# Kernel optimization log

Measured on AMD Instinct MI355X. Metric: run time of the kernel, lower is better.

## Reference

```python
import jax, jax.numpy as jnp
import numpy as np

NUM_HEADS = 12

def setup_inputs() -> dict:
    key = jax.random.key(0)
    k1, k2, k3 = jax.random.split(key, 3)
    B, N, C = 2, 4096, 768
    x = jax.random.normal(k1, (B, N, C), dtype=jnp.float32)
    w_qkv = jax.random.normal(k2, (C, 3 * C), dtype=jnp.float32) * 0.02
    b_qkv = jnp.zeros((3 * C,), dtype=jnp.float32)
    w_proj = jax.random.normal(k3, (C, C), dtype=jnp.float32) * 0.02
    b_proj = jnp.zeros((C,), dtype=jnp.float32)
    return {"x": x, "w_qkv": w_qkv, "b_qkv": b_qkv, "w_proj": w_proj, "b_proj": b_proj}

def reference(x, w_qkv, b_qkv, w_proj, b_proj):
    B, N, C = x.shape
    H = NUM_HEADS
    D = C // H
    # fused QKV projection: [B,N,3C] -> [B,N,3,H,D] -> [3,B,H,N,D]
    qkv = (x @ w_qkv + b_qkv).reshape(B, N, 3, H, D).transpose(2, 0, 3, 1, 4)
    q, k, v = qkv[0], qkv[1], qkv[2]
    # unnormalized (softmax-free) attention, same op order as the torch module
    attn = jnp.einsum('bhnd,bhmd->bhnm', q, k) / jnp.sqrt(jnp.float32(D))  # [B,H,N,N]
    out = jnp.einsum('bhnm,bhmd->bhnd', attn, v)  # [B,H,N,D]
    out = out.transpose(0, 2, 1, 3).reshape(B, N, C)
    return out @ w_proj + b_proj
```

## Files before the change

### kernel.cpp

```cpp
#include <hip/hip_runtime.h>

typedef unsigned short ushort_t;
typedef __bf16 bf16_t;
typedef __attribute__((ext_vector_type(8))) bf16_t bf16x8;
typedef __attribute__((ext_vector_type(4))) float f32x4;

__device__ __forceinline__ ushort_t f2bf(float f) {
  unsigned int u = __builtin_bit_cast(unsigned int, f);
  u += 0x7FFFu + ((u >> 16) & 1u);
  return (ushort_t)(u >> 16);
}

__device__ __forceinline__ float bf2f(ushort_t s) {
  return __builtin_bit_cast(float, (unsigned int)s << 16);
}

__device__ __forceinline__ f32x4 mfma16(bf16x8 a, bf16x8 b, f32x4 c) {
  return __builtin_amdgcn_mfma_f32_16x16x32_bf16(a, b, c, 0, 0, 0);
}

__device__ __forceinline__ void async_copy16(const void* g, void* l) {
  __builtin_amdgcn_global_load_lds(
      (const __attribute__((address_space(1))) unsigned int*)g,
      (__attribute__((address_space(3))) unsigned int*)l,
      16, 0, 0);
}

#define BARRIER { __builtin_amdgcn_s_barrier(); asm volatile("" ::: "memory"); }
#define VMW3 asm volatile("s_waitcnt vmcnt(3)" ::: "memory")
#define VMW0 asm volatile("s_waitcnt vmcnt(0)" ::: "memory")

__global__ __launch_bounds__(256) void conv_all_k(const float* __restrict__ x,
                                                  const float* __restrict__ w,
                                                  ushort_t* __restrict__ xb,
                                                  ushort_t* __restrict__ wqt,
                                                  ushort_t* __restrict__ wqr) {
  __shared__ float lds[64][65];
  const int bid = blockIdx.x;
  const int tid = threadIdx.x;
  if (bid < 3072) {
    int i = (bid * 256 + tid) * 8;
    float4 f0 = *(const float4*)(x + i);
    float4 f1 = *(const float4*)(x + i + 4);
    union { ushort_t s[8]; uint4 v; } u;
    u.s[0] = f2bf(f0.x); u.s[1] = f2bf(f0.y); u.s[2] = f2bf(f0.z); u.s[3] = f2bf(f0.w);
    u.s[4] = f2bf(f1.x); u.s[5] = f2bf(f1.y); u.s[6] = f2bf(f1.z); u.s[7] = f2bf(f1.w);
    *(uint4*)(xb + i) = u.v;
  } else if (bid < 3360) {
    const int ii = bid - 3072;
    const int n0 = 768 + (ii % 24) * 64;
    const int k0 = (ii / 24) * 64;
#pragma unroll
    for (int q = 0; q < 16; ++q) {
      int lin = tid + q * 256;
      int i = lin >> 6, j = lin & 63;
      lds[i][j] = w[(size_t)(k0 + i) * 2304 + n0 + j];
    }
    __syncthreads();
#pragma unroll
    for (int q = 0; q < 16; ++q) {
      int lin = tid + q * 256;
      int jj = lin >> 6, kk = lin & 63;
      wqt[(size_t)(n0 + jj) * 768 + k0 + kk] = f2bf(lds[kk][jj]);
    }
  } else {
    int i = ((bid - 3360) * 256 + tid) * 8;
    int row = i / 768, col = i % 768;
    const float* src = w + (size_t)row * 2304 + col;
    float4 f0 = *(const float4*)src;
    float4 f1 = *(const float4*)(src + 4);
    union { ushort_t s[8]; uint4 v; } u;
    u.s[0] = f2bf(f0.x); u.s[1] = f2bf(f0.y); u.s[2] = f2bf(f0.z); u.s[3] = f2bf(f0.w);
    u.s[4] = f2bf(f1.x); u.s[5] = f2bf(f1.y); u.s[6] = f2bf(f1.z); u.s[7] = f2bf(f1.w);
    *(uint4*)(wqr + i) = u.v;
  }
}

template <bool OUT_BF16>
__global__ __launch_bounds__(512, 2) void g256x192_k(
    const ushort_t* __restrict__ A, int lda, long long sA,
    const ushort_t* __restrict__ Bt, int ldb, long long sB,
    const float* __restrict__ bias, long long sBias,
    void* __restrict__ Cp, int ldc, long long sC,
    int K, int ntiles) {
  __shared__ char smem[114688];
  const int tid = threadIdx.x;
  const int lane = tid & 63;
  const int wid = tid >> 6;
  const int l15 = lane & 15, lhi = lane >> 4;
  const int wr = wid >> 2, wc = wid & 3;
  const int sx = l15 & 7;

  const int nwg = gridDim.x;
  const int q = nwg >> 3;
  const int swz = (blockIdx.x & 7) * q + (blockIdx.x >> 3);
  const int mt = swz / ntiles, nt = swz % ntiles;
  const int m0 = mt << 8, n0 = nt * 192;
  const long long z = blockIdx.y;

  const ushort_t* Ab = A + z * sA;
  const ushort_t* Bb = Bt + z * sB;

  const int r0 = tid >> 3;
  const int sg = tid & 7;
  const int soff = (sg ^ (r0 & 7)) << 4;

#define STAGE_A(BUF, H, K0)                                                      \
  { const char* g0 = (const char*)(Ab + (size_t)(m0 + (H)*128 + r0) * lda + (K0)) + soff;      \
    const char* g1 = (const char*)(Ab + (size_t)(m0 + (H)*128 + r0 + 64) * lda + (K0)) + soff; \
    char* lb = smem + (BUF)*57344 + (H)*16384;                                   \
    async_copy16(g0, lb + tid * 16);                                             \
    async_copy16(g1, lb + 8192 + tid * 16); }

#define STAGE_B3(BUF, J, K0)                                                     \
  { const char* g0 = (const char*)(Bb + (size_t)(n0 + (J)*64 + r0) * ldb + (K0)) + soff;       \
    async_copy16(g0, smem + (BUF)*57344 + 32768 + (J)*8192 + tid * 16); }

  const int aBase = wr * 16384 + l15 * 128;
  const int bBase = 32768 + (wc * 48 + l15) * 128;
  const int sk0 = ((lhi ^ sx) << 4);
  const int sk1 = (((4 + lhi) ^ sx) << 4);

  f32x4 acc[8][3] = {};
  bf16x8 bfr[3][2];

#define DS_A(BUF, MPAIR, AF)                                                     \
  _Pragma("unroll") for (int mm = 0; mm < 2; ++mm) {                             \
    AF[mm][0] = *(const bf16x8*)(smem + (BUF)*57344 + aBase + ((MPAIR)*2+mm)*2048 + sk0); \
    AF[mm][1] = *(const bf16x8*)(smem + (BUF)*57344 + aBase + ((MPAIR)*2+mm)*2048 + sk1); }

#define DS_B(BUF)                                                                \
  _Pragma("unroll") for (int n = 0; n < 3; ++n) {                                \
    bfr[n][0] = *(const bf16x8*)(smem + (BUF)*57344 + bBase + n*2048 + sk0);     \
    bfr[n][1] = *(const bf16x8*)(smem + (BUF)*57344 + bBase + n*2048 + sk1); }

#define MFMA_PH(MPAIR, AF)                                                       \
  __builtin_amdgcn_s_setprio(1);                                                 \
  _Pragma("unroll") for (int mm = 0; mm < 2; ++mm)                               \
    _Pragma("unroll") for (int n = 0; n < 3; ++n) {                              \
      acc[(MPAIR)*2+mm][n] = mfma16(AF[mm][0], bfr[n][0], acc[(MPAIR)*2+mm][n]); \
      acc[(MPAIR)*2+mm][n] = mfma16(AF[mm][1], bfr[n][1], acc[(MPAIR)*2+mm][n]); } \
  __builtin_amdgcn_s_setprio(0);

  STAGE_A(0, 0, 0) STAGE_A(0, 1, 0)
  STAGE_B3(0, 0, 0) STAGE_B3(0, 1, 0) STAGE_B3(0, 2, 0)
  STAGE_B3(1, 0, 64) STAGE_B3(1, 1, 64) STAGE_B3(1, 2, 64)
  VMW3;
  BARRIER

  const int NIT = K >> 7;
#pragma unroll 1
  for (int it = 0; it < NIT - 1; ++it) {
    const int kA = (it << 7) + 64;
    const int k2 = (it << 7) + 128;
    const int k3 = (it << 7) + 192;
    { bf16x8 af[2][2]; DS_B(0) DS_A(0, 0, af) STAGE_A(1, 0, kA)
      BARRIER MFMA_PH(0, af) BARRIER }
    { bf16x8 af[2][2]; DS_A(0, 1, af) STAGE_A(1, 1, kA)
      BARRIER MFMA_PH(1, af) BARRIER }
    { bf16x8 af[2][2]; DS_A(0, 2, af) STAGE_B3(0, 0, k2) STAGE_B3(0, 1, k2)
      BARRIER MFMA_PH(2, af) BARRIER }
    { bf16x8 af[2][2]; DS_A(0, 3, af) STAGE_B3(0, 2, k2) VMW3;
      BARRIER MFMA_PH(3, af) BARRIER }
    { bf16x8 af[2][2]; DS_B(1) DS_A(1, 0, af) STAGE_A(0, 0, k2)
      BARRIER MFMA_PH(0, af) BARRIER }
    { bf16x8 af[2][2]; DS_A(1, 1, af) STAGE_A(0, 1, k2)
      BARRIER MFMA_PH(1, af) BARRIER }
    { bf16x8 af[2][2]; DS_A(1, 2, af) STAGE_B3(1, 0, k3) STAGE_B3(1, 1, k3)
      BARRIER MFMA_PH(2, af) BARRIER }
    { bf16x8 af[2][2]; DS_A(1, 3, af) STAGE_B3(1, 2, k3) VMW3;
      BARRIER MFMA_PH(3, af) BARRIER }
  }
  {
    const int kA = ((NIT - 1) << 7) + 64;
    { bf16x8 af[2][2]; DS_B(0) DS_A(0, 0, af) STAGE_A(1, 0, kA)
      BARRIER MFMA_PH(0, af) BARRIER }
    { bf16x8 af[2][2]; DS_A(0, 1, af) STAGE_A(1, 1, kA)
      BARRIER MFMA_PH(1, af) BARRIER }
    { bf16x8 af[2][2]; DS_A(0, 2, af)
      BARRIER MFMA_PH(2, af) BARRIER }
    { bf16x8 af[2][2]; DS_A(0, 3, af) VMW0;
      BARRIER MFMA_PH(3, af) BARRIER }
    { bf16x8 af[2][2]; DS_B(1) DS_A(1, 0, af)
      BARRIER MFMA_PH(0, af) BARRIER }
    { bf16x8 af[2][2]; DS_A(1, 1, af)
      BARRIER MFMA_PH(1, af) BARRIER }
    { bf16x8 af[2][2]; DS_A(1, 2, af)
      BARRIER MFMA_PH(2, af) BARRIER }
    { bf16x8 af[2][2]; DS_A(1, 3, af)
      BARRIER MFMA_PH(3, af) BARRIER }
  }

  float bv[3];
#pragma unroll
  for (int n = 0; n < 3; ++n) bv[n] = bias[z * sBias + n0 + wc * 48 + n * 16 + l15];
#pragma unroll
  for (int m = 0; m < 8; ++m) {
#pragma unroll
    for (int n = 0; n < 3; ++n) {
#pragma unroll
      for (int ri = 0; ri < 4; ++ri) {
        int row = m0 + wr * 128 + m * 16 + lhi * 4 + ri;
        int col = n0 + wc * 48 + n * 16 + l15;
        float v = acc[m][n][ri] + bv[n];
        size_t ci = (size_t)z * sC + (size_t)row * ldc + col;
        if (OUT_BF16) ((ushort_t*)Cp)[ci] = f2bf(v);
        else          ((float*)Cp)[ci]    = v;
      }
    }
  }
#undef STAGE_A
#undef STAGE_B3
#undef DS_A
#undef DS_B
#undef MFMA_PH
}

template <bool OUT_BF16>
__global__ __launch_bounds__(512, 2) void g128x192_k(
    const ushort_t* __restrict__ A, int lda, long long sA,
    const ushort_t* __restrict__ Bt, int ldb, long long sB,
    const float* __restrict__ bias, long long sBias,
    void* __restrict__ Cp, int ldc, long long sC,
    int K, int ntiles) {
  __shared__ char smem[81920];
  const int tid = threadIdx.x;
  const int lane = tid & 63;
  const int wid = tid >> 6;
  const int l15 = lane & 15, lhi = lane >> 4;
  const int wr = wid >> 2, wc = wid & 3;
  const int sx = l15 & 7;

  const int nwg = gridDim.x;
  const int q = nwg >> 3;
  const int swz = (blockIdx.x & 7) * q + (blockIdx.x >> 3);
  const int mt = swz / ntiles, nt = swz % ntiles;
  const int m0 = mt << 7, n0 = nt * 192;
  const long long z = blockIdx.y;

  const ushort_t* Ab = A + z * sA;
  const ushort_t* Bb = Bt + z * sB;

  const int r0 = tid >> 3;
  const int sg = tid & 7;
  const int soff = (sg ^ (r0 & 7)) << 4;

#define STAGE_A1(BUF, K0)                                                        \
  { const char* g0 = (const char*)(Ab + (size_t)(m0 + r0) * lda + (K0)) + soff;               \
    const char* g1 = (const char*)(Ab + (size_t)(m0 + r0 + 64) * lda + (K0)) + soff;          \
    char* lb = smem + (BUF)*40960;                                               \
    async_copy16(g0, lb + tid * 16);                                             \
    async_copy16(g1, lb + 8192 + tid * 16); }

#define STAGE_B3(BUF, J, K0)                                                     \
  { const char* g0 = (const char*)(Bb + (size_t)(n0 + (J)*64 + r0) * ldb + (K0)) + soff;       \
    async_copy16(g0, smem + (BUF)*40960 + 16384 + (J)*8192 + tid * 16); }

  const int aBase = wr * 8192 + l15 * 128;
  const int bBase = 16384 + (wc * 48 + l15) * 128;
  const int sk0 = ((lhi ^ sx) << 4);
  const int sk1 = (((4 + lhi) ^ sx) << 4);

  f32x4 acc[4][3] = {};
  bf16x8 bfr[3][2];

#define DS_A1(BUF, M, AF)                                                        \
  { AF[0] = *(const bf16x8*)(smem + (BUF)*40960 + aBase + (M)*2048 + sk0);       \
    AF[1] = *(const bf16x8*)(smem + (BUF)*40960 + aBase + (M)*2048 + sk1); }

#define DS_B1(BUF)                                                               \
  _Pragma("unroll") for (int n = 0; n < 3; ++n) {                                \
    bfr[n][0] = *(const bf16x8*)(smem + (BUF)*40960 + bBase + n*2048 + sk0);     \
    bfr[n][1] = *(const bf16x8*)(smem + (BUF)*40960 + bBase + n*2048 + sk1); }

#define MFMA_PH1(M, AF)                                                          \
  __builtin_amdgcn_s_setprio(1);                                                 \
  _Pragma("unroll") for (int n = 0; n < 3; ++n) {                                \
    acc[M][n] = mfma16(AF[0], bfr[n][0], acc[M][n]);                             \
    acc[M][n] = mfma16(AF[1], bfr[n][1], acc[M][n]); }                           \
  __builtin_amdgcn_s_setprio(0);

  STAGE_A1(0, 0)
  STAGE_B3(0, 0, 0) STAGE_B3(0, 1, 0) STAGE_B3(0, 2, 0)
  STAGE_B3(1, 0, 64) STAGE_B3(1, 1, 64) STAGE_B3(1, 2, 64)
  VMW3;
  BARRIER

  const int NIT = K >> 7;
#pragma unroll 1
  for (int it = 0; it < NIT - 1; ++it) {
    const int kA = (it << 7) + 64;
    const int k2 = (it << 7) + 128;
    const int k3 = (it << 7) + 192;
    { bf16x8 af[2]; DS_B1(0) DS_A1(0, 0, af) STAGE_A1(1, kA)
      BARRIER MFMA_PH1(0, af) BARRIER }
    { bf16x8 af[2]; DS_A1(0, 1, af)
      BARRIER MFMA_PH1(1, af) BARRIER }
    { bf16x8 af[2]; DS_A1(0, 2, af) STAGE_B3(0, 0, k2) STAGE_B3(0, 1, k2)
      BARRIER MFMA_PH1(2, af) BARRIER }
    { bf16x8 af[2]; DS_A1(0, 3, af) STAGE_B3(0, 2, k2) VMW3;
      BARRIER MFMA_PH1(3, af) BARRIER }
    { bf16x8 af[2]; DS_B1(1) DS_A1(1, 0, af) STAGE_A1(0, k2)
      BARRIER MFMA_PH1(0, af) BARRIER }
    { bf16x8 af[2]; DS_A1(1, 1, af)
      BARRIER MFMA_PH1(1, af) BARRIER }
    { bf16x8 af[2]; DS_A1(1, 2, af) STAGE_B3(1, 0, k3) STAGE_B3(1, 1, k3)
      BARRIER MFMA_PH1(2, af) BARRIER }
    { bf16x8 af[2]; DS_A1(1, 3, af) STAGE_B3(1, 2, k3) VMW3;
      BARRIER MFMA_PH1(3, af) BARRIER }
  }
  {
    const int kA = ((NIT - 1) << 7) + 64;
    { bf16x8 af[2]; DS_B1(0) DS_A1(0, 0, af) STAGE_A1(1, kA)
      BARRIER MFMA_PH1(0, af) BARRIER }
    { bf16x8 af[2]; DS_A1(0, 1, af)
      BARRIER MFMA_PH1(1, af) BARRIER }
    { bf16x8 af[2]; DS_A1(0, 2, af)
      BARRIER MFMA_PH1(2, af) BARRIER }
    { bf16x8 af[2]; DS_A1(0, 3, af) VMW0;
      BARRIER MFMA_PH1(3, af) BARRIER }
    { bf16x8 af[2]; DS_B1(1) DS_A1(1, 0, af)
      BARRIER MFMA_PH1(0, af) BARRIER }
    { bf16x8 af[2]; DS_A1(1, 1, af)
      BARRIER MFMA_PH1(1, af) BARRIER }
    { bf16x8 af[2]; DS_A1(1, 2, af)
      BARRIER MFMA_PH1(2, af) BARRIER }
    { bf16x8 af[2]; DS_A1(1, 3, af)
      BARRIER MFMA_PH1(3, af) BARRIER }
  }

  float bv[3];
#pragma unroll
  for (int n = 0; n < 3; ++n) bv[n] = bias[z * sBias + n0 + wc * 48 + n * 16 + l15];
#pragma unroll
  for (int m = 0; m < 4; ++m) {
#pragma unroll
    for (int n = 0; n < 3; ++n) {
#pragma unroll
      for (int ri = 0; ri < 4; ++ri) {
        int row = m0 + wr * 64 + m * 16 + lhi * 4 + ri;
        int col = n0 + wc * 48 + n * 16 + l15;
        float v = acc[m][n][ri] + bv[n];
        size_t ci = (size_t)z * sC + (size_t)row * ldc + col;
        if (OUT_BF16) ((ushort_t*)Cp)[ci] = f2bf(v);
        else          ((float*)Cp)[ci]    = v;
      }
    }
  }
#undef STAGE_A1
#undef STAGE_B3
#undef DS_A1
#undef DS_B1
#undef MFMA_PH1
}

__global__ __launch_bounds__(256) void kv_k(const ushort_t* __restrict__ kv,
                                            float* __restrict__ Sp) {
  __shared__ ushort_t kt[64][34];
  __shared__ ushort_t vt[64][34];
  const int bh = blockIdx.x;
  const int chunk = blockIdx.y;
  const int b = bh / 12, h = bh % 12;
  const size_t base = (size_t)b * 4096 * 1536;
  const int koff = h * 64, voff = 768 + h * 64;
  const int tid = threadIdx.x;
  const int d = tid & 63, ng = (tid >> 6) * 8;
  const int w = tid >> 6, l = tid & 63, l15 = l & 15, lhi = l >> 4;

  f32x4 acc[4] = {};
  const int nbeg = chunk * 256;
  for (int n0 = nbeg; n0 < nbeg + 256; n0 += 32) {
    __syncthreads();
#pragma unroll
    for (int j = 0; j < 8; ++j) {
      int nn = ng + j;
      size_t rowb = base + (size_t)(n0 + nn) * 1536;
      kt[d][nn] = kv[rowb + koff + d];
      vt[d][nn] = kv[rowb + voff + d];
    }
    __syncthreads();
    bf16x8 af = *(const bf16x8*)&kt[w * 16 + l15][lhi * 8];
#pragma unroll
    for (int t = 0; t < 4; ++t) {
      bf16x8 bf = *(const bf16x8*)&vt[t * 16 + l15][lhi * 8];
      acc[t] = mfma16(af, bf, acc[t]);
    }
  }
#pragma unroll
  for (int t = 0; t < 4; ++t) {
#pragma unroll
    for (int r = 0; r < 4; ++r) {
      int d1 = w * 16 + lhi * 4 + r;
      int d2 = t * 16 + l15;
      Sp[((size_t)chunk * 24 + bh) * 4096 + d1 * 64 + d2] = acc[t][r];
    }
  }
}

__global__ __launch_bounds__(256) void sred_k(const float* __restrict__ Sp,
                                              ushort_t* __restrict__ S) {
  int i = blockIdx.x * 256 + threadIdx.x;
  float a = 0.f;
#pragma unroll
  for (int c = 0; c < 16; ++c) a += Sp[(size_t)c * 98304 + i];
  S[i] = f2bf(a * 0.125f);
}

__global__ __launch_bounds__(256) void t_gemm_k(const ushort_t* __restrict__ S,
                                                const float* __restrict__ wproj,
                                                ushort_t* __restrict__ Tt) {
  __shared__ ushort_t a_lds[64][66];
  __shared__ ushort_t b_lds[64][66];
  const int n0 = blockIdx.x * 64;
  const int bh = blockIdx.y;
  const int b = bh / 12, h = bh % 12;
  const int tid = threadIdx.x;
  {
    int m = tid >> 2, kg = tid & 3;
#pragma unroll
    for (int j = 0; j < 16; ++j) {
      int k = kg * 16 + j;
      a_lds[m][k] = S[(size_t)bh * 4096 + m * 64 + k];
    }
    int n = tid & 63, kg2 = tid >> 6;
#pragma unroll
    for (int j = 0; j < 16; ++j) {
      int k = kg2 * 16 + j;
      b_lds[n][k] = f2bf(wproj[(size_t)(h * 64 + k) * 768 + n0 + n]);
    }
  }
  __syncthreads();
  const int w = tid >> 6, l = tid & 63, l15 = l & 15, lhi = l >> 4;
  f32x4 acc[4] = {};
#pragma unroll
  for (int kk = 0; kk < 64; kk += 32) {
    bf16x8 af = *(const bf16x8*)&a_lds[w * 16 + l15][kk + lhi * 8];
#pragma unroll
    for (int t = 0; t < 4; ++t) {
      bf16x8 bf = *(const bf16x8*)&b_lds[t * 16 + l15][kk + lhi * 8];
      acc[t] = mfma16(af, bf, acc[t]);
    }
  }
#pragma unroll
  for (int t = 0; t < 4; ++t) {
#pragma unroll
    for (int r = 0; r < 4; ++r) {
      int row = h * 64 + w * 16 + lhi * 4 + r;
      int col = n0 + t * 16 + l15;
      Tt[(size_t)b * 768 * 768 + (size_t)col * 768 + row] = f2bf(acc[t][r]);
    }
  }
}

__global__ __launch_bounds__(256) void ugcv_k(const ushort_t* __restrict__ Tt,
                                              const ushort_t* __restrict__ wqr,
                                              const float* __restrict__ bq,
                                              const float* __restrict__ bproj,
                                              ushort_t* __restrict__ Ut,
                                              float* __restrict__ cvec) {
  __shared__ ushort_t a_lds[64][72];
  __shared__ ushort_t b_lds[64][72];
  const int bid = blockIdx.x;
  const int tid = threadIdx.x;
  if (bid < 288) {
    const int n0 = (bid % 12) * 64, m0 = ((bid / 12) % 12) * 64;
    const long long z = bid / 144;
    const ushort_t* Ab = Tt + z * 768 * 768;
    const int w = tid >> 6, l = tid & 63, l15 = l & 15, lhi = l >> 4;
    const int r2 = tid >> 3, kc = (tid & 7) * 8;
    f32x4 acc[4] = {};
    for (int k0 = 0; k0 < 768; k0 += 64) {
      __syncthreads();
      *(uint4*)&a_lds[r2][kc]      = *(const uint4*)(Ab + (size_t)(m0 + r2) * 768 + k0 + kc);
      *(uint4*)&a_lds[r2 + 32][kc] = *(const uint4*)(Ab + (size_t)(m0 + r2 + 32) * 768 + k0 + kc);
      *(uint4*)&b_lds[r2][kc]      = *(const uint4*)(wqr + (size_t)(n0 + r2) * 768 + k0 + kc);
      *(uint4*)&b_lds[r2 + 32][kc] = *(const uint4*)(wqr + (size_t)(n0 + r2 + 32) * 768 + k0 + kc);
      __syncthreads();
#pragma unroll
      for (int kk = 0; kk < 2; ++kk) {
        bf16x8 af = *(const bf16x8*)&a_lds[w * 16 + l15][kk * 32 + lhi * 8];
#pragma unroll
        for (int t = 0; t < 4; ++t) {
          bf16x8 bf = *(const bf16x8*)&b_lds[t * 16 + l15][kk * 32 + lhi * 8];
          acc[t] = mfma16(af, bf, acc[t]);
        }
      }
    }
#pragma unroll
    for (int t = 0; t < 4; ++t) {
#pragma unroll
      for (int r = 0; r < 4; ++r) {
        int row = m0 + w * 16 + lhi * 4 + r, col = n0 + t * 16 + l15;
        Ut[z * 768 * 768 + (size_t)row * 768 + col] = f2bf(acc[t][r]);
      }
    }
  } else {
    const int row = (bid - 288) * 4 + (tid >> 6);
    const int lane = tid & 63;
    const ushort_t* r = Tt + (size_t)row * 768;
    float acc = 0.f;
#pragma unroll
    for (int k0 = 0; k0 < 768; k0 += 256) {
      int k = k0 + lane * 4;
      float4 b4 = *(const float4*)(bq + k);
      union { unsigned long long v; ushort_t s[4]; } u;
      u.v = *(const unsigned long long*)(r + k);
      acc += b4.x * bf2f(u.s[0]) + b4.y * bf2f(u.s[1]) +
             b4.z * bf2f(u.s[2]) + b4.w * bf2f(u.s[3]);
    }
#pragma unroll
    for (int off = 32; off > 0; off >>= 1) acc += __shfl_down(acc, off, 64);
    if (lane == 0) cvec[row] = acc + bproj[row % 768];
  }
}

extern "C" void kernel_launch(void* const* d_in, const int* in_sizes, int n_in,
                              void* d_out, int out_size, void* d_ws, size_t ws_size,
                              hipStream_t stream) {
  const float* x      = (const float*)d_in[0];
  const float* w_qkv  = (const float*)d_in[1];
  const float* b_qkv  = (const float*)d_in[2];
  const float* w_proj = (const float*)d_in[3];
  const float* b_proj = (const float*)d_in[4];
  float* out = (float*)d_out;

  char* ws = (char*)d_ws;
  ushort_t* xb   = (ushort_t*)ws;
  ushort_t* wqt  = (ushort_t*)(ws + 12582912);
  ushort_t* wqr  = (ushort_t*)(ws + 16121856);
  ushort_t* Ut   = (ushort_t*)(ws + 17301504);
  ushort_t* kv   = (ushort_t*)(ws + 19660800);
  float*    Sp   = (float*)   (ws + 44826624);
  ushort_t* S    = (ushort_t*)(ws + 51118080);
  ushort_t* Tt   = (ushort_t*)(ws + 51314688);
  float*    cvec = (float*)   (ws + 53673984);

  conv_all_k<<<dim3(3648), 256, 0, stream>>>(x, w_qkv, xb, wqt, wqr);
  g256x192_k<true><<<dim3(256, 1), 512, 0, stream>>>(
      xb, 768, 0LL, wqt + 768 * 768, 768, 0LL, b_qkv + 768, 0LL,
      kv, 1536, 0LL, 768, 8);
  kv_k<<<dim3(24, 16), 256, 0, stream>>>(kv, Sp);
  sred_k<<<dim3(384), 256, 0, stream>>>(Sp, S);
  t_gemm_k<<<dim3(12, 24), 256, 0, stream>>>(S, w_proj, Tt);
  ugcv_k<<<dim3(672), 256, 0, stream>>>(Tt, wqr, b_qkv, b_proj, Ut, cvec);
  g128x192_k<false><<<dim3(128, 2), 512, 0, stream>>>(
      xb, 768, 4096LL * 768, Ut, 768, 768LL * 768, cvec, 768LL,
      out, 768, 4096LL * 768, 768, 4);
}
```

Before: 79.07 us.

## Write K/V transposed from QKV GEMM, load directly in kv kernel, fuse reduction

The K/V projection GEMM is specialized with constant sizes and now stages its output through LDS to write K and V in a transposed (feature-major, token-contiguous) layout with 16-byte stores. The K^T V kernel then reads contiguous bf16x8 fragments straight from global memory instead of transposing through shared memory with scalar loads. The partial-sum reduction kernel is removed and folded into the T GEMM's A-tile load. This saves one launch and the uncoalesced scalar gathers, but the kv kernel now issues uncached global loads per MFMA and the T GEMM blocks each redo the 16-way reduction.

```diff
diff --git a/kernel.cpp b/kernel.cpp
--- a/kernel.cpp
+++ b/kernel.cpp
@@ -76,13 +76,9 @@
   }
 }
 
-template <bool OUT_BF16>
-__global__ __launch_bounds__(512, 2) void g256x192_k(
-    const ushort_t* __restrict__ A, int lda, long long sA,
-    const ushort_t* __restrict__ Bt, int ldb, long long sB,
-    const float* __restrict__ bias, long long sBias,
-    void* __restrict__ Cp, int ldc, long long sC,
-    int K, int ntiles) {
+__global__ __launch_bounds__(512, 2) void gkv_k(
+    const ushort_t* __restrict__ A, const ushort_t* __restrict__ Bt,
+    const float* __restrict__ bias, ushort_t* __restrict__ kvt) {
   __shared__ char smem[114688];
   const int tid = threadIdx.x;
   const int lane = tid & 63;
@@ -91,29 +87,23 @@
   const int wr = wid >> 2, wc = wid & 3;
   const int sx = l15 & 7;
 
-  const int nwg = gridDim.x;
-  const int q = nwg >> 3;
-  const int swz = (blockIdx.x & 7) * q + (blockIdx.x >> 3);
-  const int mt = swz / ntiles, nt = swz % ntiles;
+  const int swz = (blockIdx.x & 7) * 32 + (blockIdx.x >> 3);
+  const int mt = swz >> 3, nt = swz & 7;
   const int m0 = mt << 8, n0 = nt * 192;
-  const long long z = blockIdx.y;
-
-  const ushort_t* Ab = A + z * sA;
-  const ushort_t* Bb = Bt + z * sB;
 
   const int r0 = tid >> 3;
   const int sg = tid & 7;
   const int soff = (sg ^ (r0 & 7)) << 4;
 
-#define STAGE_A(BUF, H, K0)                                                      \
-  { const char* g0 = (const char*)(Ab + (size_t)(m0 + (H)*128 + r0) * lda + (K0)) + soff;      \
-    const char* g1 = (const char*)(Ab + (size_t)(m0 + (H)*128 + r0 + 64) * lda + (K0)) + soff; \
+#define KSTAGE_A(BUF, H, K0)                                                     \
+  { const char* g0 = (const char*)(A + (size_t)(m0 + (H)*128 + r0) * 768 + (K0)) + soff;      \
+    const char* g1 = (const char*)(A + (size_t)(m0 + (H)*128 + r0 + 64) * 768 + (K0)) + soff; \
     char* lb = smem + (BUF)*57344 + (H)*16384;                                   \
     async_copy16(g0, lb + tid * 16);                                             \
     async_copy16(g1, lb + 8192 + tid * 16); }
 
-#define STAGE_B3(BUF, J, K0)                                                     \
-  { const char* g0 = (const char*)(Bb + (size_t)(n0 + (J)*64 + r0) * ldb + (K0)) + soff;       \
+#define KSTAGE_B3(BUF, J, K0)                                                    \
+  { const char* g0 = (const char*)(Bt + (size_t)(n0 + (J)*64 + r0) * 768 + (K0)) + soff;       \
     async_copy16(g0, smem + (BUF)*57344 + 32768 + (J)*8192 + tid * 16); }
 
   const int aBase = wr * 16384 + l15 * 128;
@@ -124,17 +114,17 @@
   f32x4 acc[8][3] = {};
   bf16x8 bfr[3][2];
 
-#define DS_A(BUF, MPAIR, AF)                                                     \
+#define KDS_A(BUF, MPAIR, AF)                                                    \
   _Pragma("unroll") for (int mm = 0; mm < 2; ++mm) {                             \
     AF[mm][0] = *(const bf16x8*)(smem + (BUF)*57344 + aBase + ((MPAIR)*2+mm)*2048 + sk0); \
     AF[mm][1] = *(const bf16x8*)(smem + (BUF)*57344 + aBase + ((MPAIR)*2+mm)*2048 + sk1); }
 
-#define DS_B(BUF)                                                                \
+#define KDS_B(BUF)                                                               \
   _Pragma("unroll") for (int n = 0; n < 3; ++n) {                                \
     bfr[n][0] = *(const bf16x8*)(smem + (BUF)*57344 + bBase + n*2048 + sk0);     \
     bfr[n][1] = *(const bf16x8*)(smem + (BUF)*57344 + bBase + n*2048 + sk1); }
 
-#define MFMA_PH(MPAIR, AF)                                                       \
+#define KMFMA_PH(MPAIR, AF)                                                      \
   __builtin_amdgcn_s_setprio(1);                                                 \
   _Pragma("unroll") for (int mm = 0; mm < 2; ++mm)                               \
     _Pragma("unroll") for (int n = 0; n < 3; ++n) {                              \
@@ -142,78 +132,87 @@
       acc[(MPAIR)*2+mm][n] = mfma16(AF[mm][1], bfr[n][1], acc[(MPAIR)*2+mm][n]); } \
   __builtin_amdgcn_s_setprio(0);
 
-  STAGE_A(0, 0, 0) STAGE_A(0, 1, 0)
-  STAGE_B3(0, 0, 0) STAGE_B3(0, 1, 0) STAGE_B3(0, 2, 0)
-  STAGE_B3(1, 0, 64) STAGE_B3(1, 1, 64) STAGE_B3(1, 2, 64)
+  KSTAGE_A(0, 0, 0) KSTAGE_A(0, 1, 0)
+  KSTAGE_B3(0, 0, 0) KSTAGE_B3(0, 1, 0) KSTAGE_B3(0, 2, 0)
+  KSTAGE_B3(1, 0, 64) KSTAGE_B3(1, 1, 64) KSTAGE_B3(1, 2, 64)
   VMW3;
   BARRIER
 
-  const int NIT = K >> 7;
 #pragma unroll 1
-  for (int it = 0; it < NIT - 1; ++it) {
+  for (int it = 0; it < 5; ++it) {
     const int kA = (it << 7) + 64;
     const int k2 = (it << 7) + 128;
     const int k3 = (it << 7) + 192;
-    { bf16x8 af[2][2]; DS_B(0) DS_A(0, 0, af) STAGE_A(1, 0, kA)
-      BARRIER MFMA_PH(0, af) BARRIER }
-    { bf16x8 af[2][2]; DS_A(0, 1, af) STAGE_A(1, 1, kA)
-      BARRIER MFMA_PH(1, af) BARRIER }
-    { bf16x8 af[2][2]; DS_A(0, 2, af) STAGE_B3(0, 0, k2) STAGE_B3(0, 1, k2)
-      BARRIER MFMA_PH(2, af) BARRIER }
-    { bf16x8 af[2][2]; DS_A(0, 3, af) STAGE_B3(0, 2, k2) VMW3;
-      BARRIER MFMA_PH(3, af) BARRIER }
-    { bf16x8 af[2][2]; DS_B(1) DS_A(1, 0, af) STAGE_A(0, 0, k2)
-      BARRIER MFMA_PH(0, af) BARRIER }
-    { bf16x8 af[2][2]; DS_A(1, 1, af) STAGE_A(0, 1, k2)
-      BARRIER MFMA_PH(1, af) BARRIER }
-    { bf16x8 af[2][2]; DS_A(1, 2, af) STAGE_B3(1, 0, k3) STAGE_B3(1, 1, k3)
-      BARRIER MFMA_PH(2, af) BARRIER }
-    { bf16x8 af[2][2]; DS_A(1, 3, af) STAGE_B3(1, 2, k3) VMW3;
-      BARRIER MFMA_PH(3, af) BARRIER }
+    { bf16x8 af[2][2]; KDS_B(0) KDS_A(0, 0, af) KSTAGE_A(1, 0, kA)
+      BARRIER KMFMA_PH(0, af) BARRIER }
+    { bf16x8 af[2][2]; KDS_A(0, 1, af) KSTAGE_A(1, 1, kA)
+      BARRIER KMFMA_PH(1, af) BARRIER }
+    { bf16x8 af[2][2]; KDS_A(0, 2, af) KSTAGE_B3(0, 0, k2) KSTAGE_B3(0, 1, k2)
+      BARRIER KMFMA_PH(2, af) BARRIER }
+    { bf16x8 af[2][2]; KDS_A(0, 3, af) KSTAGE_B3(0, 2, k2) VMW3;
+      BARRIER KMFMA_PH(3, af) BARRIER }
+    { bf16x8 af[2][2]; KDS_B(1) KDS_A(1, 0, af) KSTAGE_A(0, 0, k2)
+      BARRIER KMFMA_PH(0, af) BARRIER }
+    { bf16x8 af[2][2]; KDS_A(1, 1, af) KSTAGE_A(0, 1, k2)
+      BARRIER KMFMA_PH(1, af) BARRIER }
+    { bf16x8 af[2][2]; KDS_A(1, 2, af) KSTAGE_B3(1, 0, k3) KSTAGE_B3(1, 1, k3)
+      BARRIER KMFMA_PH(2, af) BARRIER }
+    { bf16x8 af[2][2]; KDS_A(1, 3, af) KSTAGE_B3(1, 2, k3) VMW3;
+      BARRIER KMFMA_PH(3, af) BARRIER }
   }
   {
-    const int kA = ((NIT - 1) << 7) + 64;
-    { bf16x8 af[2][2]; DS_B(0) DS_A(0, 0, af) STAGE_A(1, 0, kA)
-      BARRIER MFMA_PH(0, af) BARRIER }
-    { bf16x8 af[2][2]; DS_A(0, 1, af) STAGE_A(1, 1, kA)
-      BARRIER MFMA_PH(1, af) BARRIER }
-    { bf16x8 af[2][2]; DS_A(0, 2, af)
-      BARRIER MFMA_PH(2, af) BARRIER }
-    { bf16x8 af[2][2]; DS_A(0, 3, af) VMW0;
-      BARRIER MFMA_PH(3, af) BARRIER }
-    { bf16x8 af[2][2]; DS_B(1) DS_A(1, 0, af)
-      BARRIER MFMA_PH(0, af) BARRIER }
-    { bf16x8 af[2][2]; DS_A(1, 1, af)
-      BARRIER MFMA_PH(1, af) BARRIER }
-    { bf16x8 af[2][2]; DS_A(1, 2, af)
-      BARRIER MFMA_PH(2, af) BARRIER }
-    { bf16x8 af[2][2]; DS_A(1, 3, af)
-      BARRIER MFMA_PH(3, af) BARRIER }
+    const int kA = (5 << 7) + 64;
+    { bf16x8 af[2][2]; KDS_B(0) KDS_A(0, 0, af) KSTAGE_A(1, 0, kA)
+      BARRIER KMFMA_PH(0, af) BARRIER }
+    { bf16x8 af[2][2]; KDS_A(0, 1, af) KSTAGE_A(1, 1, kA)
+      BARRIER KMFMA_PH(1, af) BARRIER }
+    { bf16x8 af[2][2]; KDS_A(0, 2, af)
+      BARRIER KMFMA_PH(2, af) BARRIER }
+    { bf16x8 af[2][2]; KDS_A(0, 3, af) VMW0;
+      BARRIER KMFMA_PH(3, af) BARRIER }
+    { bf16x8 af[2][2]; KDS_B(1) KDS_A(1, 0, af)
+      BARRIER KMFMA_PH(0, af) BARRIER }
+    { bf16x8 af[2][2]; KDS_A(1, 1, af)
+      BARRIER KMFMA_PH(1, af) BARRIER }
+    { bf16x8 af[2][2]; KDS_A(1, 2, af)
+      BARRIER KMFMA_PH(2, af) BARRIER }
+    { bf16x8 af[2][2]; KDS_A(1, 3, af)
+      BARRIER KMFMA_PH(3, af) BARRIER }
   }
 
   float bv[3];
 #pragma unroll
-  for (int n = 0; n < 3; ++n) bv[n] = bias[z * sBias + n0 + wc * 48 + n * 16 + l15];
+  for (int n = 0; n < 3; ++n) bv[n] = bias[n0 + wc * 48 + n * 16 + l15];
 #pragma unroll
   for (int m = 0; m < 8; ++m) {
 #pragma unroll
     for (int n = 0; n < 3; ++n) {
-#pragma unroll
-      for (int ri = 0; ri < 4; ++ri) {
-        int row = m0 + wr * 128 + m * 16 + lhi * 4 + ri;
-        int col = n0 + wc * 48 + n * 16 + l15;
-        float v = acc[m][n][ri] + bv[n];
-        size_t ci = (size_t)z * sC + (size_t)row * ldc + col;
-        if (OUT_BF16) ((ushort_t*)Cp)[ci] = f2bf(v);
-        else          ((float*)Cp)[ci]    = v;
-      }
-    }
-  }
-#undef STAGE_A
-#undef STAGE_B3
-#undef DS_A
-#undef DS_B
-#undef MFMA_PH
+      int c = wc * 48 + n * 16 + l15;
+      int r = wr * 128 + m * 16 + lhi * 4;
+      uint2 pk;
+      pk.x = (unsigned)f2bf(acc[m][n][0] + bv[n]) |
+             ((unsigned)f2bf(acc[m][n][1] + bv[n]) << 16);
+      pk.y = (unsigned)f2bf(acc[m][n][2] + bv[n]) |
+             ((unsigned)f2bf(acc[m][n][3] + bv[n]) << 16);
+      *(uint2*)(smem + c * 528 + r * 2) = pk;
+    }
+  }
+  __syncthreads();
+  const int b = m0 >> 12;
+  const int nbase = m0 & 4095;
+  ushort_t* ob = kvt + (size_t)b * 1536 * 4096;
+#pragma unroll
+  for (int p = 0; p < 12; ++p) {
+    int idx = p * 512 + tid;
+    int c = idx >> 5, rg = idx & 31;
+    uint4 v = *(const uint4*)(smem + c * 528 + rg * 16);
+    *(uint4*)(ob + (size_t)(n0 + c) * 4096 + nbase + rg * 8) = v;
+  }
+#undef KSTAGE_A
+#undef KSTAGE_B3
+#undef KDS_A
+#undef KDS_B
+#undef KMFMA_PH
 }
 
 template <bool OUT_BF16>
@@ -354,59 +353,37 @@
 #undef MFMA_PH1
 }
 
-__global__ __launch_bounds__(256) void kv_k(const ushort_t* __restrict__ kv,
-                                            float* __restrict__ Sp) {
-  __shared__ ushort_t kt[64][34];
-  __shared__ ushort_t vt[64][34];
+__global__ __launch_bounds__(256) void kvk2_k(const ushort_t* __restrict__ kvt,
+                                              float* __restrict__ Sp) {
   const int bh = blockIdx.x;
   const int chunk = blockIdx.y;
   const int b = bh / 12, h = bh % 12;
-  const size_t base = (size_t)b * 4096 * 1536;
-  const int koff = h * 64, voff = 768 + h * 64;
+  const ushort_t* Kb = kvt + (size_t)b * 1536 * 4096 + (size_t)(h * 64) * 4096;
+  const ushort_t* Vb = Kb + (size_t)768 * 4096;
   const int tid = threadIdx.x;
-  const int d = tid & 63, ng = (tid >> 6) * 8;
-  const int w = tid >> 6, l = tid & 63, l15 = l & 15, lhi = l >> 4;
+  const int w = tid >> 6, l15 = tid & 15, lhi = (tid & 63) >> 4;
+  const int nbeg = chunk * 256 + lhi * 8;
 
   f32x4 acc[4] = {};
-  const int nbeg = chunk * 256;
-  for (int n0 = nbeg; n0 < nbeg + 256; n0 += 32) {
-    __syncthreads();
-#pragma unroll
-    for (int j = 0; j < 8; ++j) {
-      int nn = ng + j;
-      size_t rowb = base + (size_t)(n0 + nn) * 1536;
-      kt[d][nn] = kv[rowb + koff + d];
-      vt[d][nn] = kv[rowb + voff + d];
-    }
-    __syncthreads();
-    bf16x8 af = *(const bf16x8*)&kt[w * 16 + l15][lhi * 8];
+  const ushort_t* ka = Kb + (size_t)(w * 16 + l15) * 4096 + nbeg;
+#pragma unroll 2
+  for (int s = 0; s < 8; ++s) {
+    bf16x8 af = *(const bf16x8*)(ka + s * 32);
 #pragma unroll
     for (int t = 0; t < 4; ++t) {
-      bf16x8 bf = *(const bf16x8*)&vt[t * 16 + l15][lhi * 8];
+      bf16x8 bf = *(const bf16x8*)(Vb + (size_t)(t * 16 + l15) * 4096 + nbeg + s * 32);
       acc[t] = mfma16(af, bf, acc[t]);
     }
   }
-#pragma unroll
-  for (int t = 0; t < 4; ++t) {
-#pragma unroll
-    for (int r = 0; r < 4; ++r) {
-      int d1 = w * 16 + lhi * 4 + r;
-      int d2 = t * 16 + l15;
-      Sp[((size_t)chunk * 24 + bh) * 4096 + d1 * 64 + d2] = acc[t][r];
-    }
-  }
-}
-
-__global__ __launch_bounds__(256) void sred_k(const float* __restrict__ Sp,
-                                              ushort_t* __restrict__ S) {
-  int i = blockIdx.x * 256 + threadIdx.x;
-  float a = 0.f;
-#pragma unroll
-  for (int c = 0; c < 16; ++c) a += Sp[(size_t)c * 98304 + i];
-  S[i] = f2bf(a * 0.125f);
-}
-
-__global__ __launch_bounds__(256) void t_gemm_k(const ushort_t* __restrict__ S,
+  float* o = Sp + ((size_t)chunk * 24 + bh) * 4096;
+#pragma unroll
+  for (int t = 0; t < 4; ++t)
+#pragma unroll
+    for (int r = 0; r < 4; ++r)
+      o[(w * 16 + lhi * 4 + r) * 64 + t * 16 + l15] = acc[t][r];
+}
+
+__global__ __launch_bounds__(256) void t_gemm_k(const float* __restrict__ Sp,
                                                 const float* __restrict__ wproj,
                                                 ushort_t* __restrict__ Tt) {
   __shared__ ushort_t a_lds[64][66];
@@ -416,11 +393,21 @@
   const int b = bh / 12, h = bh % 12;
   const int tid = threadIdx.x;
   {
-    int m = tid >> 2, kg = tid & 3;
-#pragma unroll
-    for (int j = 0; j < 16; ++j) {
-      int k = kg * 16 + j;
-      a_lds[m][k] = S[(size_t)bh * 4096 + m * 64 + k];
+    int m = tid >> 2, kq = tid & 3;
+    const float* sb = Sp + (size_t)bh * 4096 + m * 64 + kq * 16;
+#pragma unroll
+    for (int j = 0; j < 4; ++j) {
+      float4 s = {0.f, 0.f, 0.f, 0.f};
+#pragma unroll
+      for (int c = 0; c < 16; ++c) {
+        float4 v = *(const float4*)(sb + (size_t)c * 98304 + j * 4);
+        s.x += v.x; s.y += v.y; s.z += v.z; s.w += v.w;
+      }
+      int k = kq * 16 + j * 4;
+      a_lds[m][k]     = f2bf(s.x * 0.125f);
+      a_lds[m][k + 1] = f2bf(s.y * 0.125f);
+      a_lds[m][k + 2] = f2bf(s.z * 0.125f);
+      a_lds[m][k + 3] = f2bf(s.w * 0.125f);
     }
     int n = tid & 63, kg2 = tid >> 6;
 #pragma unroll
@@ -529,19 +516,15 @@
   ushort_t* wqt  = (ushort_t*)(ws + 12582912);
   ushort_t* wqr  = (ushort_t*)(ws + 16121856);
   ushort_t* Ut   = (ushort_t*)(ws + 17301504);
-  ushort_t* kv   = (ushort_t*)(ws + 19660800);
+  ushort_t* kvt  = (ushort_t*)(ws + 19660800);
   float*    Sp   = (float*)   (ws + 44826624);
-  ushort_t* S    = (ushort_t*)(ws + 51118080);
   ushort_t* Tt   = (ushort_t*)(ws + 51314688);
   float*    cvec = (float*)   (ws + 53673984);
 
   conv_all_k<<<dim3(3648), 256, 0, stream>>>(x, w_qkv, xb, wqt, wqr);
-  g256x192_k<true><<<dim3(256, 1), 512, 0, stream>>>(
-      xb, 768, 0LL, wqt + 768 * 768, 768, 0LL, b_qkv + 768, 0LL,
-      kv, 1536, 0LL, 768, 8);
-  kv_k<<<dim3(24, 16), 256, 0, stream>>>(kv, Sp);
-  sred_k<<<dim3(384), 256, 0, stream>>>(Sp, S);
-  t_gemm_k<<<dim3(12, 24), 256, 0, stream>>>(S, w_proj, Tt);
+  gkv_k<<<dim3(256, 1), 512, 0, stream>>>(xb, wqt + 768 * 768, b_qkv + 768, kvt);
+  kvk2_k<<<dim3(24, 16), 256, 0, stream>>>(kvt, Sp);
+  t_gemm_k<<<dim3(12, 24), 256, 0, stream>>>(Sp, w_proj, Tt);
   ugcv_k<<<dim3(672), 256, 0, stream>>>(Tt, wqr, b_qkv, b_proj, Ut, cvec);
   g128x192_k<false><<<dim3(128, 2), 512, 0, stream>>>(
       xb, 768, 4096LL * 768, Ut, 768, 768LL * 768, cvec, 768LL,
```

New measurement: 104.2 us. +31.8%, slower.
